# Kernel optimization log

Measured on AMD Instinct MI355X. Metric: run time of the kernel, lower is better.

The kernel has to match this reference:

```python
import jax, jax.numpy as jnp
import numpy as np

B, T, C, HEAD = 8, 4096, 64, 64

def setup_inputs() -> dict:
    key = jax.random.key(0)
    kx, kk, kq, kv = jax.random.split(key, 4)
    x = jax.random.normal(kx, (B, T, C), dtype=jnp.float32)
    # nn.Linear(n_embd, head_size, bias=False) weight has shape (head_size, n_embd)
    s = 1.0 / np.sqrt(C)
    Wk = jax.random.uniform(kk, (HEAD, C), dtype=jnp.float32, minval=-s, maxval=s)
    Wq = jax.random.uniform(kq, (HEAD, C), dtype=jnp.float32, minval=-s, maxval=s)
    Wv = jax.random.uniform(kv, (HEAD, C), dtype=jnp.float32, minval=-s, maxval=s)
    return {"x": x, "Wk": Wk, "Wq": Wq, "Wv": Wv}

def reference(x, Wk, Wq, Wv):
    Bq, Tq, Cq = x.shape
    k = jnp.einsum('btc,hc->bth', x, Wk)   # (B,T,head)
    q = jnp.einsum('btc,hc->bth', x, Wq)
    v = jnp.einsum('btc,hc->bth', x, Wv)
    scale = Cq ** (-0.5)                    # note: scales by input dim C, as in source
    wei = jnp.einsum('bth,bsh->bts', q, k) * scale  # (B,T,T)
    causal = jnp.tril(jnp.ones((Tq, Tq), dtype=bool))
    wei = jnp.where(causal, wei, -jnp.inf)
    wei = jax.nn.softmax(wei, axis=-1)      # dropout p=0.0 -> no-op
    out = jnp.einsum('bts,bsh->bth', wei, v)
    return out
```

## Files before the change

### kernel.cpp

```cpp
#include <hip/hip_runtime.h>
#include <hip/hip_bf16.h>
#include <math.h>

#define BB 8
#define TT 4096
#define HD 64

typedef __attribute__((ext_vector_type(8))) short short8;
typedef __attribute__((ext_vector_type(4))) float f32x4;
typedef __attribute__((ext_vector_type(16))) float f32x16;
typedef __attribute__((ext_vector_type(2))) unsigned int uint2v;
typedef __attribute__((ext_vector_type(4))) unsigned int uint4v;

#define LOG2E 1.44269504088896f

__device__ __forceinline__ unsigned pack_bf2(float a, float b) {
    unsigned r;
    asm("v_cvt_pk_bf16_f32 %0, %1, %2" : "=v"(r) : "v"(a), "v"(b));
    return r;
}
__device__ __forceinline__ unsigned short bfbits(float f) {
    unsigned r;
    asm("v_cvt_pk_bf16_f32 %0, %1, %2" : "=v"(r) : "v"(f), "v"(f));
    return (unsigned short)r;
}
__device__ __forceinline__ float bf2f(unsigned short u) {
    unsigned v = (unsigned)u << 16;
    return __builtin_bit_cast(float, v);
}
__device__ __forceinline__ float fexp2(float x) {
    return __builtin_amdgcn_exp2f(x);
}
__device__ __forceinline__ short8 cvt8(float4 a, float4 b, float sc) {
    uint4v u;
    u[0] = pack_bf2(a.x * sc, a.y * sc);
    u[1] = pack_bf2(a.z * sc, a.w * sc);
    u[2] = pack_bf2(b.x * sc, b.y * sc);
    u[3] = pack_bf2(b.z * sc, b.w * sc);
    return __builtin_bit_cast(short8, u);
}

__global__ __launch_bounds__(256) void qkv_proj_mfma(
    const float* __restrict__ x,
    const float* __restrict__ Wk, const float* __restrict__ Wq, const float* __restrict__ Wv,
    unsigned short* __restrict__ qo, unsigned short* __restrict__ ko,
    unsigned short* __restrict__ vto)
{
    __shared__ short lds[26112];
    short* xls = lds;
    short* wls = lds + 8192;

    const int tid = threadIdx.x;
    const int l = tid & 63, w = tid >> 6;
    const int hi = l >> 5, c31 = l & 31;
    const long t0 = (long)blockIdx.x * 128;
    const int b = (int)(t0 >> 12);
    const int tl0 = (int)(t0 & 4095);

#pragma unroll
    for (int i = 0; i < 4; ++i) {
        int slot = tid + 256 * i;
        int row = slot >> 3, bl = slot & 7;
        const float* xp = x + (t0 + row) * 64 + 8 * bl;
        float4 a = *(const float4*)xp;
        float4 bq = *(const float4*)(xp + 4);
        *(short8*)&xls[row * 64 + 8 * (bl ^ (row & 7))] = cvt8(a, bq, 1.f);
    }
#pragma unroll
    for (int i = 0; i < 6; ++i) {
        int slot = tid + 256 * i;
        int row = slot >> 3, bl = slot & 7;
        const float* wp;
        float sc;
        if (row < 64)       { wp = Wq + row * 64;         sc = 0.125f * LOG2E; }
        else if (row < 128) { wp = Wk + (row - 64) * 64;  sc = 1.f; }
        else                { wp = Wv + (row - 128) * 64; sc = 1.f; }
        wp += 8 * bl;
        float4 a = *(const float4*)wp;
        float4 bq = *(const float4*)(wp + 4);
        *(short8*)&wls[row * 64 + 8 * (bl ^ (row & 7))] = cvt8(a, bq, sc);
    }
    __syncthreads();

    short8 xf[4];
#pragma unroll
    for (int ki = 0; ki < 4; ++ki) {
        int row = 32 * w + c31;
        xf[ki] = *(const short8*)&xls[row * 64 + 8 * ((2 * ki + hi) ^ (row & 7))];
    }
    f32x16 cqk[4] = {};
#pragma unroll
    for (int nt = 0; nt < 4; ++nt) {
#pragma unroll
        for (int ki = 0; ki < 4; ++ki) {
            int row = 32 * nt + c31;
            short8 wf = *(const short8*)&wls[row * 64 + 8 * ((2 * ki + hi) ^ (row & 7))];
            cqk[nt] = __builtin_amdgcn_mfma_f32_32x32x16_bf16(xf[ki], wf, cqk[nt], 0, 0, 0);
        }
    }
    f32x16 cv[2] = {};
#pragma unroll
    for (int rt = 0; rt < 2; ++rt) {
#pragma unroll
        for (int ki = 0; ki < 4; ++ki) {
            int row = 128 + 32 * rt + c31;
            short8 wf = *(const short8*)&wls[row * 64 + 8 * ((2 * ki + hi) ^ (row & 7))];
            cv[rt] = __builtin_amdgcn_mfma_f32_32x32x16_bf16(wf, xf[ki], cv[rt], 0, 0, 0);
        }
    }

    __syncthreads();
    short* cb = lds;
    short* vb = lds + 17408;
#pragma unroll
    for (int nt = 0; nt < 4; ++nt) {
#pragma unroll
        for (int r = 0; r < 16; ++r) {
            int trow = 32 * w + (r & 3) + 8 * (r >> 2) + 4 * hi;
            cb[trow * 136 + 32 * nt + c31] = (short)bfbits(cqk[nt][r]);
        }
    }
#pragma unroll
    for (int rt = 0; rt < 2; ++rt) {
#pragma unroll
        for (int r = 0; r < 16; ++r) {
            int h = 32 * rt + (r & 3) + 8 * (r >> 2) + 4 * hi;
            vb[h * 136 + 32 * w + c31] = (short)bfbits(cv[rt][r]);
        }
    }
    __syncthreads();
    {
        int row = tid >> 1, seg = tid & 1;
        const short8* cp = (const short8*)&cb[row * 136 + seg * 64];
        unsigned short* dst = (seg == 0 ? qo : ko) + (t0 + row) * 64;
#pragma unroll
        for (int i = 0; i < 8; ++i) ((short8*)dst)[i] = cp[i];
    }
#pragma unroll
    for (int i = 0; i < 4; ++i) {
        int slot = tid + 256 * i;
        int h = slot >> 4, tc = slot & 15;
        short8 vv = *(const short8*)&vb[h * 136 + 8 * tc];
        *(short8*)(vto + ((long)b * 64 + h) * 4096 + tl0 + 8 * tc) = vv;
    }
}

__global__ __launch_bounds__(256, 4) void attn_mfma(
    const unsigned short* __restrict__ qg,
    const unsigned short* __restrict__ kg,
    const unsigned short* __restrict__ vtg,
    unsigned short* __restrict__ Opart,
    float2* __restrict__ ml,
    float* __restrict__ outg,
    int sh, int CPB)
{
    __shared__ short kls[2][4096];
    __shared__ short vls[2][4096];

    const int CT = 1 << sh;
    const int tid = threadIdx.x;
    const int l = tid & 63, w = tid >> 6;
    const int q = l & 31, hi = l >> 5;
    const int qs7 = q & 7;

    const int bid = blockIdx.x;
    const int b = bid & 7;
    const int j = bid >> 3;
    int qt = 0, ci = 0;
    {
        int acc = 0;
        for (int qq = 31; qq >= 0; --qq) {
            int nc = (2 * qq + 1 + CT) >> sh;
            if (j < acc + nc) { qt = qq; ci = j - acc; break; }
            acc += nc;
        }
    }
    const int nch = (2 * qt + 1 + CT) >> sh;
    int ntile = 2 * qt + 2 - CT * ci;
    if (ntile > CT) ntile = CT;
    const int c0 = (ci * CT) << 6;

    const int q0w = qt * 128 + 32 * w;
    const int qr = q0w + q;
    const int lastg = (q0w + 31) >> 6;

    const unsigned short* qb = qg + ((long)b * TT + qr) * HD;
    short8 qf[4];
#pragma unroll
    for (int ki = 0; ki < 4; ++ki) qf[ki] = *(const short8*)(qb + 16 * ki + 8 * hi);

    int ofs[2][4];
#pragma unroll
    for (int a = 0; a < 2; ++a)
#pragma unroll
        for (int i2 = 0; i2 < 4; ++i2)
            ofs[a][i2] = (32 * a + q) * 128 + 16 * ((2 * i2 + hi) ^ qs7);

    f32x16 oacc[2] = {};
    float m = -INFINITY, lsum = 0.f;

    const unsigned short* kbase = kg + (long)b * TT * HD;
    const unsigned short* vbase = vtg + (long)b * HD * TT;

    const int r8 = l >> 3;
    const int blsw = (l & 7) ^ r8;
    const long koff0 = (long)(8 * w + r8) * HD + 8 * blsw;
    const long voff0 = (long)(8 * w + r8) * TT + 8 * blsw;

#define STAGE(buf_, s_) do {                                                            \
    _Pragma("unroll")                                                                   \
    for (int c_ = 0; c_ < 2; ++c_) {                                                    \
        const unsigned short* kp_ = kbase + (long)(s_) * HD + koff0 + (long)c_ * 32 * HD; \
        const unsigned short* vp_ = vbase + (s_) + voff0 + (long)c_ * 32 * TT;          \
        short* kd_ = &kls[buf_][2048 * c_ + 512 * w];                                   \
        short* vd_ = &vls[buf_][2048 * c_ + 512 * w];                                   \
        __builtin_amdgcn_global_load_lds((const __attribute__((address_space(1))) void*)kp_, \
                                         (__attribute__((address_space(3))) void*)kd_, 16, 0, 0); \
        __builtin_amdgcn_global_load_lds((const __attribute__((address_space(1))) void*)vp_, \
                                         (__attribute__((address_space(3))) void*)vd_, 16, 0, 0); \
    }                                                                                   \
} while (0)

    STAGE(0, c0);

    int cur = 0;
    for (int it = 0; it < ntile; ++it) {
        const int s0 = c0 + (it << 6);
        __syncthreads();
        if (it + 1 < ntile) STAGE(cur ^ 1, s0 + 64);

        if (s0 <= q0w + 31) {
            const int gti = ci * CT + it;
            const int nkt = (gti == lastg && (w & 1) == 0) ? 1 : 2;
            const short* kb_ = kls[cur];
            const short* vb_ = vls[cur];

            f32x16 sacc[2] = {};
            __builtin_amdgcn_s_setprio(1);
#pragma unroll
            for (int kt = 0; kt < 2; ++kt) {
                if (kt < nkt) {
#pragma unroll
                    for (int ki = 0; ki < 4; ++ki) {
                        short8 kf = *(const short8*)((const char*)kb_ + ofs[kt][ki]);
                        sacc[kt] = __builtin_amdgcn_mfma_f32_32x32x16_bf16(kf, qf[ki], sacc[kt], 0, 0, 0);
                    }
                }
            }
            __builtin_amdgcn_s_setprio(0);

            if (gti == lastg) {
#pragma unroll
                for (int kt = 0; kt < 2; ++kt) {
                    if (kt >= nkt) continue;
#pragma unroll
                    for (int r = 0; r < 16; ++r) {
                        int kkg = s0 + 32 * kt + (r & 3) + 8 * (r >> 2) + 4 * hi;
                        if (kkg > qr) sacc[kt][r] = -INFINITY;
                    }
                }
            }

            float t8[8];
#pragma unroll
            for (int r = 0; r < 8; ++r) {
                float a = fmaxf(sacc[0][r], sacc[0][r + 8]);
                if (nkt == 2) a = fmaxf(a, fmaxf(sacc[1][r], sacc[1][r + 8]));
                t8[r] = a;
            }
            float pmax = fmaxf(fmaxf(fmaxf(t8[0], t8[1]), fmaxf(t8[2], t8[3])),
                               fmaxf(fmaxf(t8[4], t8[5]), fmaxf(t8[6], t8[7])));
            if (__any(pmax > m + 11.0f)) {
                pmax = fmaxf(pmax, __shfl_xor(pmax, 32, 64));
                float mn = fmaxf(m, pmax);
                float fac = fexp2(m - mn);
                lsum *= fac;
                oacc[0] *= fac;
                oacc[1] *= fac;
                m = mn;
            }

            float rsum = 0.f;
            unsigned ulo[8], uhi[8];
#pragma unroll
            for (int kt = 0; kt < 2; ++kt) {
#pragma unroll
                for (int jj = 0; jj < 4; ++jj) {
                    if (kt < nkt) {
                        float p0 = fexp2(sacc[kt][4 * jj + 0] - m);
                        float p1 = fexp2(sacc[kt][4 * jj + 1] - m);
                        float p2 = fexp2(sacc[kt][4 * jj + 2] - m);
                        float p3 = fexp2(sacc[kt][4 * jj + 3] - m);
                        rsum += (p0 + p1) + (p2 + p3);
                        ulo[4 * kt + jj] = pack_bf2(p0, p1);
                        uhi[4 * kt + jj] = pack_bf2(p2, p3);
                    } else {
                        ulo[4 * kt + jj] = 0;
                        uhi[4 * kt + jj] = 0;
                    }
                }
            }
            lsum += rsum;

            const int nks = 2 * nkt;
#pragma unroll
            for (int ks = 0; ks < 4; ++ks) {
                if (ks >= nks) continue;
                uint2v rlo = __builtin_amdgcn_permlane32_swap(ulo[2 * ks], ulo[2 * ks + 1], false, false);
                uint2v rhi = __builtin_amdgcn_permlane32_swap(uhi[2 * ks], uhi[2 * ks + 1], false, false);
                uint4v paw;
                paw[0] = rlo[0]; paw[1] = rhi[0]; paw[2] = rlo[1]; paw[3] = rhi[1];
                short8 pa = __builtin_bit_cast(short8, paw);
                __builtin_amdgcn_s_setprio(1);
#pragma unroll
                for (int dt = 0; dt < 2; ++dt) {
                    short8 vf = *(const short8*)((const char*)vb_ + ofs[dt][ks]);
                    oacc[dt] = __builtin_amdgcn_mfma_f32_32x32x16_bf16(vf, pa, oacc[dt], 0, 0, 0);
                }
                __builtin_amdgcn_s_setprio(0);
            }
        }
        cur ^= 1;
    }
#undef STAGE

    lsum += __shfl_xor(lsum, 32, 64);

    const int lr = 32 * w + q;
    if (nch == 1) {
        const float inv = 1.f / lsum;
        float* op = outg + ((long)b * TT + qr) * HD;
#pragma unroll
        for (int dt = 0; dt < 2; ++dt) {
#pragma unroll
            for (int jj = 0; jj < 4; ++jj) {
                f32x4 o4;
                o4[0] = oacc[dt][4 * jj + 0] * inv;
                o4[1] = oacc[dt][4 * jj + 1] * inv;
                o4[2] = oacc[dt][4 * jj + 2] * inv;
                o4[3] = oacc[dt][4 * jj + 3] * inv;
                *(f32x4*)(op + 32 * dt + 8 * jj + 4 * hi) = o4;
            }
        }
    } else {
        const float inv = lsum > 0.f ? 1.f / lsum : 0.f;
        unsigned short* po = Opart + ((long)(b * CPB + j) * 128 + lr) * 64;
#pragma unroll
        for (int dt = 0; dt < 2; ++dt) {
#pragma unroll
            for (int jj = 0; jj < 4; ++jj) {
                uint2v u;
                u[0] = pack_bf2(oacc[dt][4 * jj + 0] * inv, oacc[dt][4 * jj + 1] * inv);
                u[1] = pack_bf2(oacc[dt][4 * jj + 2] * inv, oacc[dt][4 * jj + 3] * inv);
                *(uint2v*)(po + 32 * dt + 8 * jj + 4 * hi) = u;
            }
        }
        ml[(long)(b * CPB + j) * 128 + lr] = make_float2(m, lsum);
    }
}

__global__ __launch_bounds__(256) void combine(
    const unsigned short* __restrict__ Opart,
    const float2* __restrict__ ml,
    float* __restrict__ outg,
    int sh, int qtmin, int CPB)
{
    const int CT = 1 << sh;
    const int bid = blockIdx.x;
    const int b = bid & 7, qt = qtmin + (bid >> 3);
    const int nc = (2 * qt + 1 + CT) >> sh;
    int jb = 0;
    for (int qq = 31; qq > qt; --qq) jb += (2 * qq + 1 + CT) >> sh;

    const int tid = threadIdx.x;
    const int row = tid >> 1, dh = (tid & 1) * 32;
    const long base = (long)(b * CPB + jb) * 128 + row;

    float mv[8], lv[8], M = -INFINITY;
#pragma unroll
    for (int c = 0; c < 8; ++c) {
        mv[c] = -INFINITY; lv[c] = 0.f;
        if (c < nc) {
            float2 t = ml[base + (long)c * 128];
            mv[c] = t.x; lv[c] = t.y;
            M = fmaxf(M, mv[c]);
        }
    }
    float L = 0.f, wt[8];
#pragma unroll
    for (int c = 0; c < 8; ++c) {
        wt[c] = (c < nc) ? lv[c] * fexp2(mv[c] - M) : 0.f;
        L += wt[c];
    }
    float acc[32];
#pragma unroll
    for (int i = 0; i < 32; ++i) acc[i] = 0.f;
#pragma unroll
    for (int c = 0; c < 8; ++c) {
        if (c < nc && wt[c] > 0.f) {
            const short8* op = (const short8*)(Opart + (base + (long)c * 128) * 64 + dh);
#pragma unroll
            for (int i = 0; i < 4; ++i) {
                short8 v = op[i];
#pragma unroll
                for (int e = 0; e < 8; ++e)
                    acc[8 * i + e] += wt[c] * bf2f((unsigned short)v[e]);
            }
        }
    }
    const float invL = 1.f / L;
    float* dst = outg + ((long)b * TT + qt * 128 + row) * HD + dh;
#pragma unroll
    for (int i = 0; i < 8; ++i) {
        f32x4 o;
        o[0] = acc[4 * i + 0] * invL; o[1] = acc[4 * i + 1] * invL;
        o[2] = acc[4 * i + 2] * invL; o[3] = acc[4 * i + 3] * invL;
        *(f32x4*)(dst + 4 * i) = o;
    }
}

extern "C" void kernel_launch(void* const* d_in, const int* in_sizes, int n_in,
                              void* d_out, int out_size, void* d_ws, size_t ws_size,
                              hipStream_t stream) {
    const float* x  = (const float*)d_in[0];
    const float* Wk = (const float*)d_in[1];
    const float* Wq = (const float*)d_in[2];
    const float* Wv = (const float*)d_in[3];
    float* out = (float*)d_out;

    const long N = (long)BB * TT * HD;
    unsigned short* q16 = (unsigned short*)d_ws;
    unsigned short* k16 = q16 + N;
    unsigned short* vt16 = k16 + N;
    const size_t qkv_bytes = 12582912;

    int sh, CPB;
    {
        const size_t need8 = qkv_bytes + (size_t)144 * 8 * 128 * 64 * 2
                                       + (size_t)144 * 8 * 128 * 8;
        if (ws_size >= need8) { sh = 3; CPB = 144; }
        else                  { sh = 4; CPB = 80;  }
    }
    unsigned short* Opart = (unsigned short*)((char*)d_ws + qkv_bytes);
    float2* mlp = (float2*)((char*)d_ws + qkv_bytes + (size_t)CPB * 8 * 128 * 64 * 2);
    const int qtmin = 1 << (sh - 1);

    qkv_proj_mfma<<<BB * TT / 128, 256, 0, stream>>>(x, Wk, Wq, Wv, q16, k16, vt16);
    attn_mfma<<<8 * CPB, 256, 0, stream>>>(q16, k16, vt16, Opart, mlp, out, sh, CPB);
    combine<<<8 * (32 - qtmin), 256, 0, stream>>>(Opart, mlp, out, sh, qtmin, CPB);
}
```

Measured before the change: 60.70 us.

## Software-pipeline QK^T of next tile with softmax/PV of previous tile

```diff
diff --git a/kernel.cpp b/kernel.cpp
--- a/kernel.cpp
+++ b/kernel.cpp
@@ -145,7 +145,7 @@
     }
 }
 
-__global__ __launch_bounds__(256, 4) void attn_mfma(
+__global__ __launch_bounds__(256, 3) void attn_mfma(
     const unsigned short* __restrict__ qg,
     const unsigned short* __restrict__ kg,
     const unsigned short* __restrict__ vtg,
@@ -154,8 +154,8 @@
     float* __restrict__ outg,
     int sh, int CPB)
 {
-    __shared__ short kls[2][4096];
-    __shared__ short vls[2][4096];
+    __shared__ short kls[3][4096];
+    __shared__ short vls[3][4096];
 
     const int CT = 1 << sh;
     const int tid = threadIdx.x;
@@ -223,106 +223,136 @@
 
     STAGE(0, c0);
 
+    f32x16 sprv0 = {}, sprv1 = {};
+    int nktp = 0, vbp = 0, pend = 0;
+
+    auto finish_prev = [&]() {
+        const short* vb_ = &vls[vbp][0];
+        float t8[8];
+#pragma unroll
+        for (int r = 0; r < 8; ++r) {
+            float a = fmaxf(sprv0[r], sprv0[r + 8]);
+            if (nktp == 2) a = fmaxf(a, fmaxf(sprv1[r], sprv1[r + 8]));
+            t8[r] = a;
+        }
+        float pmax = fmaxf(fmaxf(fmaxf(t8[0], t8[1]), fmaxf(t8[2], t8[3])),
+                           fmaxf(fmaxf(t8[4], t8[5]), fmaxf(t8[6], t8[7])));
+        if (__any(pmax > m + 11.0f)) {
+            pmax = fmaxf(pmax, __shfl_xor(pmax, 32, 64));
+            float mn = fmaxf(m, pmax);
+            float fac = fexp2(m - mn);
+            lsum *= fac;
+            oacc[0] *= fac;
+            oacc[1] *= fac;
+            m = mn;
+        }
+        float rsum = 0.f;
+        unsigned ulo[8], uhi[8];
+#pragma unroll
+        for (int jj = 0; jj < 4; ++jj) {
+            float p0 = fexp2(sprv0[4 * jj + 0] - m);
+            float p1 = fexp2(sprv0[4 * jj + 1] - m);
+            float p2 = fexp2(sprv0[4 * jj + 2] - m);
+            float p3 = fexp2(sprv0[4 * jj + 3] - m);
+            rsum += (p0 + p1) + (p2 + p3);
+            ulo[jj] = pack_bf2(p0, p1);
+            uhi[jj] = pack_bf2(p2, p3);
+        }
+        if (nktp == 2) {
+#pragma unroll
+            for (int jj = 0; jj < 4; ++jj) {
+                float p0 = fexp2(sprv1[4 * jj + 0] - m);
+                float p1 = fexp2(sprv1[4 * jj + 1] - m);
+                float p2 = fexp2(sprv1[4 * jj + 2] - m);
+                float p3 = fexp2(sprv1[4 * jj + 3] - m);
+                rsum += (p0 + p1) + (p2 + p3);
+                ulo[4 + jj] = pack_bf2(p0, p1);
+                uhi[4 + jj] = pack_bf2(p2, p3);
+            }
+        } else {
+#pragma unroll
+            for (int jj = 0; jj < 4; ++jj) { ulo[4 + jj] = 0; uhi[4 + jj] = 0; }
+        }
+        lsum += rsum;
+        const int nks = 2 * nktp;
+#pragma unroll
+        for (int ks = 0; ks < 4; ++ks) {
+            if (ks >= nks) continue;
+            uint2v rlo = __builtin_amdgcn_permlane32_swap(ulo[2 * ks], ulo[2 * ks + 1], false, false);
+            uint2v rhi = __builtin_amdgcn_permlane32_swap(uhi[2 * ks], uhi[2 * ks + 1], false, false);
+            uint4v paw;
+            paw[0] = rlo[0]; paw[1] = rhi[0]; paw[2] = rlo[1]; paw[3] = rhi[1];
+            short8 pa = __builtin_bit_cast(short8, paw);
+            __builtin_amdgcn_s_setprio(1);
+#pragma unroll
+            for (int dt = 0; dt < 2; ++dt) {
+                short8 vf = *(const short8*)((const char*)vb_ + ofs[dt][ks]);
+                oacc[dt] = __builtin_amdgcn_mfma_f32_32x32x16_bf16(vf, pa, oacc[dt], 0, 0, 0);
+            }
+            __builtin_amdgcn_s_setprio(0);
+        }
+    };
+
     int cur = 0;
     for (int it = 0; it < ntile; ++it) {
         const int s0 = c0 + (it << 6);
         __syncthreads();
-        if (it + 1 < ntile) STAGE(cur ^ 1, s0 + 64);
-
-        if (s0 <= q0w + 31) {
+        const int nx = (cur == 2) ? 0 : cur + 1;
+        if (it + 1 < ntile) STAGE(nx, s0 + 64);
+
+        const bool doCur = (s0 <= q0w + 31);
+        f32x16 scur0 = {}, scur1 = {};
+        int nktc = 2;
+        if (doCur) {
             const int gti = ci * CT + it;
-            const int nkt = (gti == lastg && (w & 1) == 0) ? 1 : 2;
-            const short* kb_ = kls[cur];
-            const short* vb_ = vls[cur];
-
-            f32x16 sacc[2] = {};
+            nktc = (gti == lastg && (w & 1) == 0) ? 1 : 2;
+            const short* kb_ = &kls[cur][0];
+
             __builtin_amdgcn_s_setprio(1);
 #pragma unroll
-            for (int kt = 0; kt < 2; ++kt) {
-                if (kt < nkt) {
-#pragma unroll
-                    for (int ki = 0; ki < 4; ++ki) {
-                        short8 kf = *(const short8*)((const char*)kb_ + ofs[kt][ki]);
-                        sacc[kt] = __builtin_amdgcn_mfma_f32_32x32x16_bf16(kf, qf[ki], sacc[kt], 0, 0, 0);
+            for (int ki = 0; ki < 4; ++ki) {
+                short8 kf = *(const short8*)((const char*)kb_ + ofs[0][ki]);
+                scur0 = __builtin_amdgcn_mfma_f32_32x32x16_bf16(kf, qf[ki], scur0, 0, 0, 0);
+            }
+            if (nktc == 2) {
+#pragma unroll
+                for (int ki = 0; ki < 4; ++ki) {
+                    short8 kf = *(const short8*)((const char*)kb_ + ofs[1][ki]);
+                    scur1 = __builtin_amdgcn_mfma_f32_32x32x16_bf16(kf, qf[ki], scur1, 0, 0, 0);
+                }
+            }
+            __builtin_amdgcn_s_setprio(0);
+        }
+
+        if (pend) { finish_prev(); pend = 0; }
+
+        if (doCur) {
+            const int gti = ci * CT + it;
+            if (gti == lastg) {
+#pragma unroll
+                for (int r = 0; r < 16; ++r) {
+                    int kkg = s0 + (r & 3) + 8 * (r >> 2) + 4 * hi;
+                    if (kkg > qr) scur0[r] = -INFINITY;
+                }
+                if (nktc == 2) {
+#pragma unroll
+                    for (int r = 0; r < 16; ++r) {
+                        int kkg = s0 + 32 + (r & 3) + 8 * (r >> 2) + 4 * hi;
+                        if (kkg > qr) scur1[r] = -INFINITY;
                     }
                 }
             }
-            __builtin_amdgcn_s_setprio(0);
-
-            if (gti == lastg) {
-#pragma unroll
-                for (int kt = 0; kt < 2; ++kt) {
-                    if (kt >= nkt) continue;
-#pragma unroll
-                    for (int r = 0; r < 16; ++r) {
-                        int kkg = s0 + 32 * kt + (r & 3) + 8 * (r >> 2) + 4 * hi;
-                        if (kkg > qr) sacc[kt][r] = -INFINITY;
-                    }
-                }
-            }
-
-            float t8[8];
-#pragma unroll
-            for (int r = 0; r < 8; ++r) {
-                float a = fmaxf(sacc[0][r], sacc[0][r + 8]);
-                if (nkt == 2) a = fmaxf(a, fmaxf(sacc[1][r], sacc[1][r + 8]));
-                t8[r] = a;
-            }
-            float pmax = fmaxf(fmaxf(fmaxf(t8[0], t8[1]), fmaxf(t8[2], t8[3])),
-                               fmaxf(fmaxf(t8[4], t8[5]), fmaxf(t8[6], t8[7])));
-            if (__any(pmax > m + 11.0f)) {
-                pmax = fmaxf(pmax, __shfl_xor(pmax, 32, 64));
-                float mn = fmaxf(m, pmax);
-                float fac = fexp2(m - mn);
-                lsum *= fac;
-                oacc[0] *= fac;
-                oacc[1] *= fac;
-                m = mn;
-            }
-
-            float rsum = 0.f;
-            unsigned ulo[8], uhi[8];
-#pragma unroll
-            for (int kt = 0; kt < 2; ++kt) {
-#pragma unroll
-                for (int jj = 0; jj < 4; ++jj) {
-                    if (kt < nkt) {
-                        float p0 = fexp2(sacc[kt][4 * jj + 0] - m);
-                        float p1 = fexp2(sacc[kt][4 * jj + 1] - m);
-                        float p2 = fexp2(sacc[kt][4 * jj + 2] - m);
-                        float p3 = fexp2(sacc[kt][4 * jj + 3] - m);
-                        rsum += (p0 + p1) + (p2 + p3);
-                        ulo[4 * kt + jj] = pack_bf2(p0, p1);
-                        uhi[4 * kt + jj] = pack_bf2(p2, p3);
-                    } else {
-                        ulo[4 * kt + jj] = 0;
-                        uhi[4 * kt + jj] = 0;
-                    }
-                }
-            }
-            lsum += rsum;
-
-            const int nks = 2 * nkt;
-#pragma unroll
-            for (int ks = 0; ks < 4; ++ks) {
-                if (ks >= nks) continue;
-                uint2v rlo = __builtin_amdgcn_permlane32_swap(ulo[2 * ks], ulo[2 * ks + 1], false, false);
-                uint2v rhi = __builtin_amdgcn_permlane32_swap(uhi[2 * ks], uhi[2 * ks + 1], false, false);
-                uint4v paw;
-                paw[0] = rlo[0]; paw[1] = rhi[0]; paw[2] = rlo[1]; paw[3] = rhi[1];
-                short8 pa = __builtin_bit_cast(short8, paw);
-                __builtin_amdgcn_s_setprio(1);
-#pragma unroll
-                for (int dt = 0; dt < 2; ++dt) {
-                    short8 vf = *(const short8*)((const char*)vb_ + ofs[dt][ks]);
-                    oacc[dt] = __builtin_amdgcn_mfma_f32_32x32x16_bf16(vf, pa, oacc[dt], 0, 0, 0);
-                }
-                __builtin_amdgcn_s_setprio(0);
-            }
-        }
-        cur ^= 1;
+            sprv0 = scur0;
+            sprv1 = scur1;
+            nktp = nktc;
+            vbp = cur;
+            pend = 1;
+        }
+        cur = nx;
     }
 #undef STAGE
+
+    if (pend) finish_prev();
 
     lsum += __shfl_xor(lsum, 32, 64);
 
```

Result: slower. 66.51 us (+9.6%).
